# Kernel tuning notes

Measured on AMD Instinct MI355X. Metric: run time of the kernel, lower is better.

The kernel has to match this reference:

```python
import jax, jax.numpy as jnp
import numpy as np

N_HEAD = 16
N_KV_GROUP = 4
WINDOW = 256


def setup_inputs() -> dict:
    key = jax.random.key(0)
    ks = jax.random.split(key, 5)
    B, T, C = 2, 2048, 1024
    KV = C // N_HEAD * N_KV_GROUP  # 256
    s = 0.02
    return {
        "x": jax.random.normal(ks[0], (B, T, C), jnp.float32),
        "Wq": jax.random.normal(ks[1], (C, C), jnp.float32) * s,
        "bq": jnp.zeros((C,), jnp.float32),
        "Wk": jax.random.normal(ks[2], (C, KV), jnp.float32) * s,
        "bk": jnp.zeros((KV,), jnp.float32),
        "Wv": jax.random.normal(ks[3], (C, KV), jnp.float32) * s,
        "bv": jnp.zeros((KV,), jnp.float32),
        "Wo": jax.random.normal(ks[4], (C, C), jnp.float32) * s,
        "bo": jnp.zeros((C,), jnp.float32),
    }


def reference(x, Wq, bq, Wk, bk, Wv, bv, Wo, bo):
    B, T, C = x.shape
    hd = C // N_HEAD  # head dim = 64
    n_rep = N_HEAD // N_KV_GROUP

    q = x @ Wq + bq                      # [B,T,C]
    k = x @ Wk + bk                      # [B,T,KV]
    v = x @ Wv + bv

    q = q.reshape(B, T, N_HEAD, hd).transpose(0, 2, 1, 3)       # [B,H,T,d]
    k = k.reshape(B, T, N_KV_GROUP, hd).transpose(0, 2, 1, 3)   # [B,G,T,d]
    v = v.reshape(B, T, N_KV_GROUP, hd).transpose(0, 2, 1, 3)

    # GQA: repeat_interleave kv heads along head dim
    k_rep = jnp.repeat(k, n_rep, axis=1)                         # [B,H,T,d]
    v_rep = jnp.repeat(v, n_rep, axis=1)

    att = jnp.einsum("bhqd,bhkd->bhqk", q, k_rep) / jnp.sqrt(jnp.float32(hd))

    # causal + sliding window band mask: q position i attends to j in [i-WINDOW, i]
    i = jnp.arange(T)[:, None]
    j = jnp.arange(T)[None, :]
    band = (j <= i) & (j >= i - WINDOW)                           # [T,T]
    att = jnp.where(band[None, None], att, jnp.float32(-jnp.inf))

    att = jax.nn.softmax(att, axis=-1)
    y = jnp.einsum("bhqk,bhkd->bhqd", att, v_rep)                 # [B,H,T,d]
    y = y.transpose(0, 2, 1, 3).reshape(B, T, C)
    return y @ Wo + bo
```

## Files before the change

### kernel.cpp

```cpp
#include <hip/hip_runtime.h>
#include <hip/hip_bf16.h>

#define TT 2048
#define CC 1024
#define KVD 256
#define QKVD 1536

typedef __bf16 bf16x8 __attribute__((ext_vector_type(8)));
typedef float f32x4 __attribute__((ext_vector_type(4)));

__device__ __forceinline__ void gload_lds16(const __hip_bfloat16* g, __hip_bfloat16* l) {
  __builtin_amdgcn_global_load_lds(
      (const __attribute__((address_space(1))) unsigned int*)g,
      (__attribute__((address_space(3))) unsigned int*)l, 16, 0, 0);
}


__global__ __launch_bounds__(256) void k_convert_x(const float* __restrict__ x,
                                                   __hip_bfloat16* __restrict__ xbf) {
  size_t idx = ((size_t)blockIdx.x * 256 + threadIdx.x) * 4;
  float4 v = *(const float4*)(x + idx);
  xbf[idx + 0] = __float2bfloat16(v.x);
  xbf[idx + 1] = __float2bfloat16(v.y);
  xbf[idx + 2] = __float2bfloat16(v.z);
  xbf[idx + 3] = __float2bfloat16(v.w);
}

__global__ __launch_bounds__(256) void k_pack_w(const float* __restrict__ Wq,
                                                const float* __restrict__ Wk,
                                                const float* __restrict__ Wv,
                                                const float* __restrict__ Wo,
                                                const float* __restrict__ bq,
                                                const float* __restrict__ bk,
                                                const float* __restrict__ bv,
                                                __hip_bfloat16* __restrict__ wqkvT,
                                                __hip_bfloat16* __restrict__ woT,
                                                float* __restrict__ bqkv) {
  if (blockIdx.z == 1 && blockIdx.y >= 16) {
    if (blockIdx.y == 16 && blockIdx.x == 0) {
      for (int i = threadIdx.x; i < 1536; i += 256) {
        float v;
        if (i < 1024)      v = bq[i];
        else if (i < 1280) v = bk[i - 1024];
        else               v = bv[i - 1280];
        bqkv[i] = v;
      }
    }
    return;
  }
  __shared__ float tile[64][65];
  const int k0 = blockIdx.x * 64;
  const int n0 = blockIdx.y * 64;
  const float* src;
  int ncols;
  __hip_bfloat16* dst;
  if (blockIdx.z == 0) {
    dst = wqkvT;
    if (n0 < 1024)      { src = Wq; ncols = 1024; }
    else if (n0 < 1280) { src = Wk - 1024; ncols = 256; }
    else                { src = Wv - 1280; ncols = 256; }
  } else {
    dst = woT; src = Wo; ncols = 1024;
  }
  const int rw = threadIdx.x >> 6;
  const int cl = threadIdx.x & 63;
#pragma unroll
  for (int i = 0; i < 16; ++i) {
    const int kr = rw + i * 4;
    tile[kr][cl] = src[(size_t)(k0 + kr) * ncols + n0 + cl];
  }
  __syncthreads();
#pragma unroll
  for (int i = 0; i < 16; ++i) {
    const int nr = rw + i * 4;
    dst[(size_t)(n0 + nr) * 1024 + k0 + cl] = __float2bfloat16(tile[cl][nr]);
  }
}

__global__ __launch_bounds__(256) void k_vT(const __hip_bfloat16* __restrict__ qkv,
                                            __hip_bfloat16* __restrict__ vtg) {
  __shared__ __hip_bfloat16 tile[64][72];
  const int t0 = blockIdx.x * 64;
  const int g  = blockIdx.y;
  const int b  = blockIdx.z;
  const int r  = threadIdx.x >> 2;
  const int c  = (threadIdx.x & 3) * 16;
  const __hip_bfloat16* src = qkv + ((size_t)(b * TT + t0 + r)) * QKVD + 1280 + g * 64 + c;
  *(uint4*)&tile[r][c]     = *(const uint4*)src;
  *(uint4*)&tile[r][c + 8] = *(const uint4*)(src + 8);
  __syncthreads();
  __hip_bfloat16 tmp[16];
#pragma unroll
  for (int u = 0; u < 16; ++u) tmp[u] = tile[c + u][r];
  __hip_bfloat16* dst = vtg + ((size_t)((b * 4 + g) * 64 + r)) * TT + t0 + c;
  *(uint4*)dst       = *(const uint4*)tmp;
  *(uint4*)(dst + 8) = *(const uint4*)(tmp + 8);
}


template <bool OUT_BF16>
__global__ __launch_bounds__(256, 4) void k_gemm_bt(const __hip_bfloat16* __restrict__ A,
                                                    const __hip_bfloat16* __restrict__ BT,
                                                    const float* __restrict__ bias,
                                                    void* __restrict__ C,
                                                    int M, int N, int K) {
  __shared__ __hip_bfloat16 As[64][64];
  __shared__ __hip_bfloat16 Bs[128][64];

  const int tid  = threadIdx.x;
  const int m0   = blockIdx.y * 64;
  const int n0   = blockIdx.x * 128;
  const int w    = tid >> 6;
  const int lane = tid & 63;
  const int quad = lane >> 4;
  const int l16  = lane & 15;
  const int wm   = (w >> 1) * 32;
  const int wn   = (w & 1) * 64;

  const int dl_r = lane >> 3;
  const int dl_c = (lane & 7) ^ dl_r;

  const __hip_bfloat16* gA = A + (size_t)(m0 + w * 16 + dl_r) * K + dl_c * 8;
  const __hip_bfloat16* gB = BT + (size_t)(n0 + w * 32 + dl_r) * K + dl_c * 8;

  f32x4 acc[2][4] = {};

  const int nk = K >> 6;
  for (int kt = 0; kt < nk; ++kt) {
    const int k0 = kt << 6;
    gload_lds16(gA + k0,                 &As[w * 16][0]);
    gload_lds16(gA + k0 + (size_t)8 * K, &As[w * 16 + 8][0]);
    gload_lds16(gB + k0,                  &Bs[w * 32][0]);
    gload_lds16(gB + k0 + (size_t)8 * K,  &Bs[w * 32 + 8][0]);
    gload_lds16(gB + k0 + (size_t)16 * K, &Bs[w * 32 + 16][0]);
    gload_lds16(gB + k0 + (size_t)24 * K, &Bs[w * 32 + 24][0]);
    __syncthreads();

#pragma unroll
    for (int ks = 0; ks < 2; ++ks) {
      const int cb = (ks << 2) + quad;
      bf16x8 fa[2], fb[4];
#pragma unroll
      for (int i = 0; i < 2; ++i)
        fa[i] = *(const bf16x8*)&As[wm + i * 16 + l16][(cb ^ (l16 & 7)) << 3];
#pragma unroll
      for (int j = 0; j < 4; ++j)
        fb[j] = *(const bf16x8*)&Bs[wn + j * 16 + l16][(cb ^ (l16 & 7)) << 3];
#pragma unroll
      for (int i = 0; i < 2; ++i)
#pragma unroll
        for (int j = 0; j < 4; ++j)
          acc[i][j] = __builtin_amdgcn_mfma_f32_16x16x32_bf16(fa[i], fb[j], acc[i][j], 0, 0, 0);
    }
    __syncthreads();
  }

#pragma unroll
  for (int j = 0; j < 4; ++j) {
    const int gn = n0 + wn + j * 16 + l16;
    const float bias_v = bias[gn];
#pragma unroll
    for (int i = 0; i < 2; ++i) {
      const int gmb = m0 + wm + i * 16 + quad * 4;
#pragma unroll
      for (int r = 0; r < 4; ++r) {
        const float v = acc[i][j][r] + bias_v;
        const size_t idx = (size_t)(gmb + r) * N + gn;
        if (OUT_BF16) ((__hip_bfloat16*)C)[idx] = __float2bfloat16(v);
        else          ((float*)C)[idx] = v;
      }
    }
  }
}


__global__ __launch_bounds__(256) void k_attn(const __hip_bfloat16* __restrict__ qkv,
                                              const __hip_bfloat16* __restrict__ vtg,
                                              __hip_bfloat16* __restrict__ y) {
  __shared__ __hip_bfloat16 Ps[4][16][72];

  const int t    = threadIdx.x;
  const int w    = t >> 6;
  const int lane = t & 63;
  const int quad = lane >> 4;
  const int l16  = lane & 15;
  const int bx   = blockIdx.x;
  const int h    = blockIdx.y;
  const int b    = blockIdx.z;
  const int g    = h >> 2;
  const int i0   = bx * 64;
  const int qrow      = i0 + w * 16 + l16;
  const int my_q_base = i0 + w * 16 + quad * 4;

  bf16x8 fq[2];
  {
    const __hip_bfloat16* qp = qkv + ((size_t)(b * TT + qrow)) * QKVD + h * 64 + quad * 8;
    fq[0] = *(const bf16x8*)qp;
    fq[1] = *(const bf16x8*)(qp + 32);
  }

  float l_r[4] = {0.f, 0.f, 0.f, 0.f};
  f32x4 o_acc[4] = {};

  const int c_lo = bx >= 4 ? bx - 4 : 0;
  const float EC = 0.125f * 1.44269504f;

  for (int c = c_lo; c <= bx; ++c) {
    const int jc = c * 64;

    bf16x8 fk[4][2];
    const __hip_bfloat16* kbase =
        qkv + ((size_t)(b * TT + jc + l16)) * QKVD + 1024 + g * 64 + quad * 8;
#pragma unroll
    for (int nt = 0; nt < 4; ++nt) {
      fk[nt][0] = *(const bf16x8*)(kbase + (size_t)nt * 16 * QKVD);
      fk[nt][1] = *(const bf16x8*)(kbase + (size_t)nt * 16 * QKVD + 32);
    }
    bf16x8 fv[4][2];
    const __hip_bfloat16* vbase =
        vtg + ((size_t)((b * 4 + g) * 64 + l16)) * TT + jc + quad * 8;
#pragma unroll
    for (int jt = 0; jt < 4; ++jt) {
      fv[jt][0] = *(const bf16x8*)(vbase + (size_t)jt * 16 * TT);
      fv[jt][1] = *(const bf16x8*)(vbase + (size_t)jt * 16 * TT + 32);
    }

    f32x4 sacc[4] = {};
#pragma unroll
    for (int nt = 0; nt < 4; ++nt) {
      sacc[nt] = __builtin_amdgcn_mfma_f32_16x16x32_bf16(fq[0], fk[nt][0], sacc[nt], 0, 0, 0);
      sacc[nt] = __builtin_amdgcn_mfma_f32_16x16x32_bf16(fq[1], fk[nt][1], sacc[nt], 0, 0, 0);
    }

#pragma unroll
    for (int r = 0; r < 4; ++r) {
      const int gi = my_q_base + r;
      const int lo = gi - 256;
#pragma unroll
      for (int nt = 0; nt < 4; ++nt) {
        const int key = jc + nt * 16 + l16;
        const bool valid = (key <= gi) & (key >= lo);
        const float p = valid ? exp2f(sacc[nt][r] * EC) : 0.f;
        l_r[r] += p;
        Ps[w][quad * 4 + r][nt * 16 + l16] = __float2bfloat16(p);
      }
    }

    bf16x8 fp0 = *(const bf16x8*)&Ps[w][l16][quad * 8];
    bf16x8 fp1 = *(const bf16x8*)&Ps[w][l16][32 + quad * 8];

#pragma unroll
    for (int jt = 0; jt < 4; ++jt) {
      o_acc[jt] = __builtin_amdgcn_mfma_f32_16x16x32_bf16(fp0, fv[jt][0], o_acc[jt], 0, 0, 0);
      o_acc[jt] = __builtin_amdgcn_mfma_f32_16x16x32_bf16(fp1, fv[jt][1], o_acc[jt], 0, 0, 0);
    }
  }

#pragma unroll
  for (int r = 0; r < 4; ++r) {
#pragma unroll
    for (int d = 1; d < 16; d <<= 1) l_r[r] += __shfl_xor(l_r[r], d);
    const float inv = 1.f / l_r[r];
    __hip_bfloat16* yp = y + ((size_t)(b * TT + my_q_base + r)) * CC + h * 64 + l16;
#pragma unroll
    for (int jt = 0; jt < 4; ++jt)
      yp[jt * 16] = __float2bfloat16(o_acc[jt][r] * inv);
  }
}


extern "C" void kernel_launch(void* const* d_in, const int* in_sizes, int n_in,
                              void* d_out, int out_size, void* d_ws, size_t ws_size,
                              hipStream_t stream) {
  const float* x  = (const float*)d_in[0];
  const float* Wq = (const float*)d_in[1];
  const float* bq = (const float*)d_in[2];
  const float* Wk = (const float*)d_in[3];
  const float* bk = (const float*)d_in[4];
  const float* Wv = (const float*)d_in[5];
  const float* bv = (const float*)d_in[6];
  const float* Wo = (const float*)d_in[7];
  const float* bo = (const float*)d_in[8];
  float* out = (float*)d_out;

  char* ws = (char*)d_ws;
  const size_t M = 2 * TT;
  __hip_bfloat16* xbf   = (__hip_bfloat16*)(ws);
  __hip_bfloat16* qkv   = (__hip_bfloat16*)(ws + 8388608);
  __hip_bfloat16* ybf   = (__hip_bfloat16*)(ws + 20971520);
  __hip_bfloat16* wqkvT = (__hip_bfloat16*)(ws + 29360128);
  __hip_bfloat16* woT   = (__hip_bfloat16*)(ws + 32505856);
  float*          bqkv  = (float*)(ws + 34603008);
  __hip_bfloat16* vtg   = (__hip_bfloat16*)(ws + 34609152);

  k_convert_x<<<4096, 256, 0, stream>>>(x, xbf);
  k_pack_w<<<dim3(16, 24, 2), 256, 0, stream>>>(Wq, Wk, Wv, Wo, bq, bk, bv,
                                                wqkvT, woT, bqkv);

  k_gemm_bt<true><<<dim3(QKVD / 128, M / 64), 256, 0, stream>>>(xbf, wqkvT, bqkv, qkv,
                                                                (int)M, QKVD, CC);
  k_vT<<<dim3(TT / 64, 4, 2), 256, 0, stream>>>(qkv, vtg);

  k_attn<<<dim3(TT / 64, 16, 2), 256, 0, stream>>>(qkv, vtg, ybf);

  k_gemm_bt<false><<<dim3(CC / 128, M / 64), 256, 0, stream>>>(ybf, woT, bo, out,
                                                               (int)M, CC, CC);
}
```

Measured before the change: 169.5 us.

## Fuse V transpose into QKV GEMM epilogue and double-buffer K/V in LDS

The QKV GEMM epilogue now writes the V columns directly in transposed layout, which removes the separate k_vT kernel launch and its extra round trip through global memory. The attention kernel now stages K and V chunks into double-buffered LDS with direct global-to-LDS loads and swizzled addressing. The next chunk is prefetched while the current one is computed, replacing per-wave redundant global fragment loads. In exchange it adds LDS usage and a block-wide barrier per chunk, and the transposed V stores are narrow 8-byte writes.

```diff
diff --git a/kernel.cpp b/kernel.cpp
--- a/kernel.cpp
+++ b/kernel.cpp
@@ -77,32 +77,13 @@
   }
 }
 
-__global__ __launch_bounds__(256) void k_vT(const __hip_bfloat16* __restrict__ qkv,
-                                            __hip_bfloat16* __restrict__ vtg) {
-  __shared__ __hip_bfloat16 tile[64][72];
-  const int t0 = blockIdx.x * 64;
-  const int g  = blockIdx.y;
-  const int b  = blockIdx.z;
-  const int r  = threadIdx.x >> 2;
-  const int c  = (threadIdx.x & 3) * 16;
-  const __hip_bfloat16* src = qkv + ((size_t)(b * TT + t0 + r)) * QKVD + 1280 + g * 64 + c;
-  *(uint4*)&tile[r][c]     = *(const uint4*)src;
-  *(uint4*)&tile[r][c + 8] = *(const uint4*)(src + 8);
-  __syncthreads();
-  __hip_bfloat16 tmp[16];
-#pragma unroll
-  for (int u = 0; u < 16; ++u) tmp[u] = tile[c + u][r];
-  __hip_bfloat16* dst = vtg + ((size_t)((b * 4 + g) * 64 + r)) * TT + t0 + c;
-  *(uint4*)dst       = *(const uint4*)tmp;
-  *(uint4*)(dst + 8) = *(const uint4*)(tmp + 8);
-}
-
-
-template <bool OUT_BF16>
+
+template <bool OUT_BF16, bool SPLIT_V>
 __global__ __launch_bounds__(256, 4) void k_gemm_bt(const __hip_bfloat16* __restrict__ A,
                                                     const __hip_bfloat16* __restrict__ BT,
                                                     const float* __restrict__ bias,
                                                     void* __restrict__ C,
+                                                    __hip_bfloat16* __restrict__ vtg,
                                                     int M, int N, int K) {
   __shared__ __hip_bfloat16 As[64][64];
   __shared__ __hip_bfloat16 Bs[128][64];
@@ -159,15 +140,31 @@
   for (int j = 0; j < 4; ++j) {
     const int gn = n0 + wn + j * 16 + l16;
     const float bias_v = bias[gn];
-#pragma unroll
-    for (int i = 0; i < 2; ++i) {
-      const int gmb = m0 + wm + i * 16 + quad * 4;
-#pragma unroll
-      for (int r = 0; r < 4; ++r) {
-        const float v = acc[i][j][r] + bias_v;
-        const size_t idx = (size_t)(gmb + r) * N + gn;
-        if (OUT_BF16) ((__hip_bfloat16*)C)[idx] = __float2bfloat16(v);
-        else          ((float*)C)[idx] = v;
+    if (SPLIT_V && gn >= 1280) {
+      const int dfull = gn - 1280;
+      const int gg = dfull >> 6;
+      const int dd = dfull & 63;
+#pragma unroll
+      for (int i = 0; i < 2; ++i) {
+        const int gm = m0 + wm + i * 16 + quad * 4;
+        const int bb = gm >> 11;
+        const int tl = gm & 2047;
+        __hip_bfloat16 tmp[4];
+#pragma unroll
+        for (int r = 0; r < 4; ++r) tmp[r] = __float2bfloat16(acc[i][j][r] + bias_v);
+        *(uint2*)(vtg + ((size_t)((bb * 4 + gg) * 64 + dd)) * TT + tl) = *(const uint2*)tmp;
+      }
+    } else {
+#pragma unroll
+      for (int i = 0; i < 2; ++i) {
+        const int gmb = m0 + wm + i * 16 + quad * 4;
+#pragma unroll
+        for (int r = 0; r < 4; ++r) {
+          const float v = acc[i][j][r] + bias_v;
+          const size_t idx = (size_t)(gmb + r) * N + gn;
+          if (OUT_BF16) ((__hip_bfloat16*)C)[idx] = __float2bfloat16(v);
+          else          ((float*)C)[idx] = v;
+        }
       }
     }
   }
@@ -177,6 +174,8 @@
 __global__ __launch_bounds__(256) void k_attn(const __hip_bfloat16* __restrict__ qkv,
                                               const __hip_bfloat16* __restrict__ vtg,
                                               __hip_bfloat16* __restrict__ y) {
+  __shared__ __hip_bfloat16 Kb[2][64][64];
+  __shared__ __hip_bfloat16 Vb[2][64][64];
   __shared__ __hip_bfloat16 Ps[4][16][72];
 
   const int t    = threadIdx.x;
@@ -192,6 +191,14 @@
   const int qrow      = i0 + w * 16 + l16;
   const int my_q_base = i0 + w * 16 + quad * 4;
 
+  const int lrow = lane >> 3;
+  const int cgl  = (lane & 7) ^ lrow;
+
+  const __hip_bfloat16* kg =
+      qkv + ((size_t)(b * TT + w * 16 + lrow)) * QKVD + 1024 + g * 64 + cgl * 8;
+  const __hip_bfloat16* vg =
+      vtg + ((size_t)((b * 4 + g) * 64 + w * 16 + lrow)) * TT + cgl * 8;
+
   bf16x8 fq[2];
   {
     const __hip_bfloat16* qp = qkv + ((size_t)(b * TT + qrow)) * QKVD + h * 64 + quad * 8;
@@ -201,35 +208,42 @@
 
   float l_r[4] = {0.f, 0.f, 0.f, 0.f};
   f32x4 o_acc[4] = {};
+  const float EC = 0.125f * 1.44269504f;
 
   const int c_lo = bx >= 4 ? bx - 4 : 0;
-  const float EC = 0.125f * 1.44269504f;
-
+
+  {
+    const size_t ko = (size_t)(c_lo * 64) * QKVD;
+    gload_lds16(kg + ko,                   &Kb[0][w * 16][0]);
+    gload_lds16(kg + ko + (size_t)8 * QKVD, &Kb[0][w * 16 + 8][0]);
+    const int vo = c_lo * 64;
+    gload_lds16(vg + vo,                  &Vb[0][w * 16][0]);
+    gload_lds16(vg + vo + (size_t)8 * TT, &Vb[0][w * 16 + 8][0]);
+  }
+
+  int buf = 0;
   for (int c = c_lo; c <= bx; ++c) {
+    __syncthreads();
+    if (c < bx) {
+      const size_t ko = (size_t)((c + 1) * 64) * QKVD;
+      gload_lds16(kg + ko,                    &Kb[buf ^ 1][w * 16][0]);
+      gload_lds16(kg + ko + (size_t)8 * QKVD, &Kb[buf ^ 1][w * 16 + 8][0]);
+      const int vo = (c + 1) * 64;
+      gload_lds16(vg + vo,                  &Vb[buf ^ 1][w * 16][0]);
+      gload_lds16(vg + vo + (size_t)8 * TT, &Vb[buf ^ 1][w * 16 + 8][0]);
+    }
+
     const int jc = c * 64;
 
-    bf16x8 fk[4][2];
-    const __hip_bfloat16* kbase =
-        qkv + ((size_t)(b * TT + jc + l16)) * QKVD + 1024 + g * 64 + quad * 8;
-#pragma unroll
-    for (int nt = 0; nt < 4; ++nt) {
-      fk[nt][0] = *(const bf16x8*)(kbase + (size_t)nt * 16 * QKVD);
-      fk[nt][1] = *(const bf16x8*)(kbase + (size_t)nt * 16 * QKVD + 32);
-    }
-    bf16x8 fv[4][2];
-    const __hip_bfloat16* vbase =
-        vtg + ((size_t)((b * 4 + g) * 64 + l16)) * TT + jc + quad * 8;
-#pragma unroll
-    for (int jt = 0; jt < 4; ++jt) {
-      fv[jt][0] = *(const bf16x8*)(vbase + (size_t)jt * 16 * TT);
-      fv[jt][1] = *(const bf16x8*)(vbase + (size_t)jt * 16 * TT + 32);
-    }
-
     f32x4 sacc[4] = {};
 #pragma unroll
-    for (int nt = 0; nt < 4; ++nt) {
-      sacc[nt] = __builtin_amdgcn_mfma_f32_16x16x32_bf16(fq[0], fk[nt][0], sacc[nt], 0, 0, 0);
-      sacc[nt] = __builtin_amdgcn_mfma_f32_16x16x32_bf16(fq[1], fk[nt][1], sacc[nt], 0, 0, 0);
+    for (int ks = 0; ks < 2; ++ks) {
+      const int sw = (((ks << 2) + quad) ^ (l16 & 7)) << 3;
+#pragma unroll
+      for (int nt = 0; nt < 4; ++nt) {
+        const bf16x8 fk = *(const bf16x8*)&Kb[buf][nt * 16 + l16][sw];
+        sacc[nt] = __builtin_amdgcn_mfma_f32_16x16x32_bf16(fq[ks], fk, sacc[nt], 0, 0, 0);
+      }
     }
 
 #pragma unroll
@@ -246,14 +260,20 @@
       }
     }
 
-    bf16x8 fp0 = *(const bf16x8*)&Ps[w][l16][quad * 8];
-    bf16x8 fp1 = *(const bf16x8*)&Ps[w][l16][32 + quad * 8];
-
-#pragma unroll
-    for (int jt = 0; jt < 4; ++jt) {
-      o_acc[jt] = __builtin_amdgcn_mfma_f32_16x16x32_bf16(fp0, fv[jt][0], o_acc[jt], 0, 0, 0);
-      o_acc[jt] = __builtin_amdgcn_mfma_f32_16x16x32_bf16(fp1, fv[jt][1], o_acc[jt], 0, 0, 0);
-    }
+    const bf16x8 fp0 = *(const bf16x8*)&Ps[w][l16][quad * 8];
+    const bf16x8 fp1 = *(const bf16x8*)&Ps[w][l16][32 + quad * 8];
+
+#pragma unroll
+    for (int ks = 0; ks < 2; ++ks) {
+      const int sw = (((ks << 2) + quad) ^ (l16 & 7)) << 3;
+#pragma unroll
+      for (int jt = 0; jt < 4; ++jt) {
+        const bf16x8 fv = *(const bf16x8*)&Vb[buf][jt * 16 + l16][sw];
+        o_acc[jt] = __builtin_amdgcn_mfma_f32_16x16x32_bf16(ks == 0 ? fp0 : fp1, fv,
+                                                            o_acc[jt], 0, 0, 0);
+      }
+    }
+    buf ^= 1;
   }
 
 #pragma unroll
@@ -297,12 +317,11 @@
   k_pack_w<<<dim3(16, 24, 2), 256, 0, stream>>>(Wq, Wk, Wv, Wo, bq, bk, bv,
                                                 wqkvT, woT, bqkv);
 
-  k_gemm_bt<true><<<dim3(QKVD / 128, M / 64), 256, 0, stream>>>(xbf, wqkvT, bqkv, qkv,
-                                                                (int)M, QKVD, CC);
-  k_vT<<<dim3(TT / 64, 4, 2), 256, 0, stream>>>(qkv, vtg);
+  k_gemm_bt<true, true><<<dim3(QKVD / 128, M / 64), 256, 0, stream>>>(
+      xbf, wqkvT, bqkv, qkv, vtg, (int)M, QKVD, CC);
 
   k_attn<<<dim3(TT / 64, 16, 2), 256, 0, stream>>>(qkv, vtg, ybf);
 
-  k_gemm_bt<false><<<dim3(CC / 128, M / 64), 256, 0, stream>>>(ybf, woT, bo, out,
-                                                               (int)M, CC, CC);
-}
+  k_gemm_bt<false, false><<<dim3(CC / 128, M / 64), 256, 0, stream>>>(
+      ybf, woT, bo, out, nullptr, (int)M, CC, CC);
+}
```

Result: faster. 147.1 us (-13.2%).
